# Kernel tuning notes

Hardware: AMD Instinct MI355X
Metric: run time of the kernel (lower is better)

The kernel has to match this reference:

```python
import jax, jax.numpy as jnp
import numpy as np

B, NV, H, W = 4, 1, 224, 224
GH = GW = 16                 # 224 // 14 patch grid
NT = 1 + GH * GW             # 257 tokens (cls + patches)
CIN, DF, DH = 1152, 512, 128
NP0 = 512
UPF = (4, 8)
RADIUS = 1.0


def setup_inputs():
    key = jax.random.key(0)
    ks = jax.random.split(key, 8)
    rn = lambda k, s, sc: jax.random.normal(k, s) * sc
    points = jax.random.uniform(ks[0], (B, NP0, 3), minval=-0.5, maxval=0.5)
    tokens = rn(ks[1], (B, CIN, NT), 0.5)
    # OpenGL-style c2w (the forward flips cols 1:3 to OpenCV); camera at z=+2 looking at origin
    c2w = np.tile(np.eye(4, dtype=np.float32), (B, NV, 1, 1))
    c2w[..., 2, 3] = 2.0
    K = np.zeros((B, NV, 3, 3), dtype=np.float32)
    K[..., 0, 0] = 250.0; K[..., 1, 1] = 250.0
    K[..., 0, 2] = W / 2.0; K[..., 1, 2] = H / 2.0
    K[..., 2, 2] = 1.0
    return dict(
        points=points, input_image_tokens=tokens,
        c2w_cond=jnp.asarray(c2w), intrinsic_cond=jnp.asarray(K),
        w1=rn(ks[2], (2 * DF, CIN), CIN ** -0.5), b1=jnp.zeros((2 * DF,)),
        w2=rn(ks[3], (DF, 2 * DF), (2 * DF) ** -0.5), b2=jnp.zeros((DF,)),
        s0_w1=rn(ks[4], (DH, 3 + DF), (3 + DF) ** -0.5), s0_b1=jnp.zeros((DH,)),
        s0_ow=rn(ks[5], (UPF[0] * 3, DH), DH ** -0.5), s0_ob=jnp.zeros((UPF[0] * 3,)),
        s1_w1=rn(ks[6], (DH, 3 + DF), (3 + DF) ** -0.5), s1_b1=jnp.zeros((DH,)),
        s1_ow=rn(ks[7], (UPF[1] * 3, DH), DH ** -0.5), s1_ob=jnp.zeros((UPF[1] * 3,)))


def _points_projection(pts, c2w, K, lf):
    # pts: (B,N,3), c2w: (B,4,4) OpenCV, K: (B,3,3), lf: (B,C,H,W)
    N = pts.shape[1]
    w2c = jnp.linalg.inv(c2w)
    cam = jnp.einsum('bij,bnj->bni', w2c[:, :3, :3], pts) + w2c[:, None, :3, 3]
    z = cam[..., 2]
    zs = jnp.where(jnp.abs(z) > 1e-8, z, 1e-8)
    px = K[:, 0, 0][:, None] * cam[..., 0] / zs + K[:, 0, 2][:, None]
    py = K[:, 1, 1][:, None] * cam[..., 1] / zs + K[:, 1, 2][:, None]
    ix = jnp.floor(px).astype(jnp.int32)
    iy = jnp.floor(py).astype(jnp.int32)
    valid = (z > 1e-6) & (ix >= 0) & (ix < W) & (iy >= 0) & (iy < H)
    pix = jnp.where(valid, iy * W + ix, H * W)                  # (B,N); dummy bin H*W
    nseg = B * (H * W + 1)
    seg = (jnp.arange(B)[:, None] * (H * W + 1) + pix).reshape(-1)
    zf = jnp.where(valid, z, jnp.inf).reshape(-1)
    minz = jax.ops.segment_min(zf, seg, num_segments=nseg)      # z-buffer (points_per_pixel=1)
    ismin = valid.reshape(-1) & (zf <= minz[seg])
    pid = jnp.arange(B * N)
    win = jax.ops.segment_min(jnp.where(ismin, pid, B * N), seg, num_segments=nseg)
    visible = (pid == win[seg]).reshape(B, N)                   # unique winner per pixel
    lff = lf.reshape(B, -1, H * W)
    g = jnp.take_along_axis(lff, jnp.clip(pix, 0, H * W - 1)[:, None, :], axis=2)  # (B,C,N)
    return jnp.where(visible[:, None, :], g, 0.0)


def reference(points, input_image_tokens, c2w_cond, intrinsic_cond,
              w1, b1, w2, b2, s0_w1, s0_b1, s0_ow, s0_ob, s1_w1, s1_b1, s1_ow, s1_ob):
    # mlp_feat_cond: 1x1 conv MLP over tokens
    feat = jax.nn.relu(jnp.einsum('oc,bcn->bon', w1, input_image_tokens) + b1[:, None])
    feat = jnp.einsum('oc,bcn->bon', w2, feat) + b2[:, None]    # (B, DF, NT)
    # OpenGL -> OpenCV flip of c2w columns 1:3
    flip = jnp.ones((4, 4)).at[:3, 1:3].set(-1.0)
    c2w = c2w_cond[:, 0] * flip
    Kmat = intrinsic_cond[:, 0]
    # drop cls token, to patch grid, bilinear upsample to image resolution
    lf = jnp.transpose(feat, (0, 2, 1))[:, 1:].reshape(B, GH, GW, DF)
    lf = jnp.transpose(lf, (0, 3, 1, 2))
    lf = jax.image.resize(lf, (B, DF, H, W), method='bilinear')  # (B, DF, H, W)
    pts = points
    pcd = jnp.transpose(points, (0, 2, 1))                      # (B,3,N)
    stages = (((s0_w1, s0_b1, s0_ow, s0_ob), UPF[0]), ((s1_w1, s1_b1, s1_ow, s1_ob), UPF[1]))
    outs = []
    for (ws, bs, ow, ob), f in stages:
        up_cond = _points_projection(pts, c2w, Kmat, lf)        # (B, DF, N) visibility-masked gather
        h = jax.nn.relu(jnp.einsum('oc,bcn->bon', ws,
                                   jnp.concatenate([pcd, up_cond], axis=1)) + bs[:, None])
        off = jnp.tanh(jnp.einsum('oc,bcn->bon', ow, h) + ob[:, None])  # (B, 3f, N)
        n = pcd.shape[2]
        off = off.reshape(B, f, 3, n).transpose(0, 2, 3, 1).reshape(B, 3, n * f)
        pcd = jnp.repeat(pcd, f, axis=2) + off * RADIUS         # SPD-style bounded upsample
        pts = jnp.transpose(pcd, (0, 2, 1))
        outs.append(pts)
    return tuple(outs)
```

## Files before the change

kernel.cpp:

```cpp
#include <hip/hip_runtime.h>
#include <hip/hip_bf16.h>
#include <cstdint>
#include <cstddef>

using bf16 = __hip_bfloat16;
typedef __attribute__((ext_vector_type(8))) short bf16x8_t;
typedef __attribute__((ext_vector_type(4))) float f32x4_t;

#define BB 4
#define HH 224
#define WWD 224
#define NTOK 257
#define CINC 1152
#define DFC 512

constexpr size_t OFF_G2    = 256;
constexpr size_t OFF_WC    = OFF_G2;
constexpr size_t OFF_T     = OFF_G2 + 1052672;
constexpr size_t OFF_SCR   = 256 + 2105344;
constexpr size_t OFF_FEAT1 = OFF_SCR;
constexpr size_t OFF_ZBUF  = OFF_SCR;
constexpr size_t OFF_PINFO = OFF_SCR + 1605632;
constexpr size_t WS_NEED   = OFF_SCR + 1736704;
constexpr size_t WS_FULL   = OFF_SCR + 4210688;

__device__ __forceinline__ float ldf(const void* p, size_t i, bool f32) {
  return f32 ? ((const float*)p)[i] : __bfloat162float(((const bf16*)p)[i]);
}
__device__ __forceinline__ double ldd(const void* p, size_t i, bool f32) {
  return f32 ? (double)((const float*)p)[i]
             : (double)__bfloat162float(((const bf16*)p)[i]);
}
__device__ __forceinline__ bool detect_f32(const void* c2w_raw) {
  const float* fc = (const float*)c2w_raw;
  return (fc[0] == 1.0f) && (fc[5] == 1.0f);
}

__device__ void compute_cam(const void* c2w_raw, const void* K_raw, int b, bool f32,
                            double* cw) {
  double m[16];
#pragma unroll
  for (int i = 0; i < 16; ++i) m[i] = ldd(c2w_raw, b*16 + i, f32);
  m[1]=-m[1]; m[2]=-m[2]; m[5]=-m[5]; m[6]=-m[6]; m[9]=-m[9]; m[10]=-m[10];
  double i0  =  m[5]*m[10]*m[15] - m[5]*m[11]*m[14] - m[9]*m[6]*m[15] + m[9]*m[7]*m[14] + m[13]*m[6]*m[11] - m[13]*m[7]*m[10];
  double i4  = -m[4]*m[10]*m[15] + m[4]*m[11]*m[14] + m[8]*m[6]*m[15] - m[8]*m[7]*m[14] - m[12]*m[6]*m[11] + m[12]*m[7]*m[10];
  double i8  =  m[4]*m[9]*m[15]  - m[4]*m[11]*m[13] - m[8]*m[5]*m[15] + m[8]*m[7]*m[13] + m[12]*m[5]*m[11] - m[12]*m[7]*m[9];
  double i12 = -m[4]*m[9]*m[14]  + m[4]*m[10]*m[13] + m[8]*m[5]*m[14] - m[8]*m[6]*m[13] - m[12]*m[5]*m[10] + m[12]*m[6]*m[9];
  double i1  = -m[1]*m[10]*m[15] + m[1]*m[11]*m[14] + m[9]*m[2]*m[15] - m[9]*m[3]*m[14] - m[13]*m[2]*m[11] + m[13]*m[3]*m[10];
  double i5  =  m[0]*m[10]*m[15] - m[0]*m[11]*m[14] - m[8]*m[2]*m[15] + m[8]*m[3]*m[14] + m[12]*m[2]*m[11] - m[12]*m[3]*m[10];
  double i9  = -m[0]*m[9]*m[15]  + m[0]*m[11]*m[13] + m[8]*m[1]*m[15] - m[8]*m[3]*m[13] - m[12]*m[1]*m[11] + m[12]*m[3]*m[9];
  double i13 =  m[0]*m[9]*m[14]  - m[0]*m[10]*m[13] - m[8]*m[1]*m[14] + m[8]*m[2]*m[13] + m[12]*m[1]*m[10] - m[12]*m[2]*m[9];
  double i2  =  m[1]*m[6]*m[15]  - m[1]*m[7]*m[14]  - m[5]*m[2]*m[15] + m[5]*m[3]*m[14] + m[13]*m[2]*m[7]  - m[13]*m[3]*m[6];
  double i6  = -m[0]*m[6]*m[15]  + m[0]*m[7]*m[14]  + m[4]*m[2]*m[15] - m[4]*m[3]*m[14] - m[12]*m[2]*m[7]  + m[12]*m[3]*m[6];
  double i10 =  m[0]*m[5]*m[15]  - m[0]*m[7]*m[13]  - m[4]*m[1]*m[15] + m[4]*m[3]*m[13] + m[12]*m[1]*m[7]  - m[12]*m[3]*m[5];
  double i14 = -m[0]*m[5]*m[14]  + m[0]*m[6]*m[13]  + m[4]*m[1]*m[14] - m[4]*m[2]*m[13] - m[12]*m[1]*m[6]  + m[12]*m[2]*m[5];
  double i3  = -m[1]*m[6]*m[11]  + m[1]*m[7]*m[10]  + m[5]*m[2]*m[11] - m[5]*m[3]*m[10] - m[9]*m[2]*m[7]   + m[9]*m[3]*m[6];
  double i7  =  m[0]*m[6]*m[11]  - m[0]*m[7]*m[10]  - m[4]*m[2]*m[11] + m[4]*m[3]*m[10] + m[8]*m[2]*m[7]   - m[8]*m[3]*m[6];
  double i11 = -m[0]*m[5]*m[11]  + m[0]*m[7]*m[9]   + m[4]*m[1]*m[11] - m[4]*m[3]*m[9]  - m[8]*m[1]*m[7]   + m[8]*m[3]*m[5];
  double det = m[0]*i0 + m[1]*i4 + m[2]*i8 + m[3]*i12;
  double r = 1.0 / det;
  cw[0]=i0*r;  cw[1]=i1*r;  cw[2]=i2*r;  cw[3]=i3*r;
  cw[4]=i4*r;  cw[5]=i5*r;  cw[6]=i6*r;  cw[7]=i7*r;
  cw[8]=i8*r;  cw[9]=i9*r;  cw[10]=i10*r; cw[11]=i11*r;
  cw[12] = ldd(K_raw, b*9+0, f32);
  cw[13] = ldd(K_raw, b*9+2, f32);
  cw[14] = ldd(K_raw, b*9+4, f32);
  cw[15] = ldd(K_raw, b*9+5, f32);
}

template <int XK, int WK, bool TROUT, bool ATOMIC, bool BSTR, int PREC>
__global__ __launch_bounds__(256) void gemm_mfma(
    const void* __restrict__ Wm, const void* __restrict__ Wm2,
    const void* __restrict__ X, const void* __restrict__ xb,
    const float* __restrict__ bstr_p, int bstr,
    float* __restrict__ Y, const void* __restrict__ c2w_raw,
    int O, int K, int Nn, int Yld,
    int bx0, int bxm, int by0, int bym,
    int Wld, int Wc0, int skn) {
  __shared__ __align__(16) short SMEM[6 * 2560];
  short* Whi = SMEM;
  short* Wmd = SMEM + 2560;
  short* Wlo = SMEM + 5120;
  short* Xhi = SMEM + 7680;
  short* Xmd = SMEM + 10240;
  short* Xlo = SMEM + 12800;
  const bool f32 = detect_f32(c2w_raw);
  int tid = threadIdx.x;
  int n0 = blockIdx.x * 64;
  int o0 = blockIdx.y * 64;
  int bz = (int)blockIdx.z;
  int bidx = bz / skn;
  int ks = bz - bidx * skn;
  int bx = bx0 + bxm * bidx;
  int by = by0 + bym * bidx;
  int kq = K / skn;
  int kbase = ks * kq;
  int so  = tid >> 2;
  int skq = tid & 3;
  int sn  = tid & 63;
  int skg = tid >> 6;
  int wv = tid >> 6, lane = tid & 63;
  int lm = lane & 15, lq = lane >> 4;

  float wreg[8], xreg[8];
  f32x4_t acc[4] = {};

  auto load_w = [&](int c0) {
    if constexpr (WK == 3) {
      int orow = o0 + so;
      const void* Wp = (orow < 128) ? Wm : Wm2;
      size_t base = (size_t)(orow & 127) * Wld + Wc0 + c0 + skq * 8;
#pragma unroll
      for (int j = 0; j < 8; ++j) wreg[j] = ldf(Wp, base + j, f32);
    } else if constexpr (WK == 1) {
      const float* Wf = (const float*)Wm;
      size_t base = (size_t)(o0 + so) * Wld + c0 + skq * 8;
      float4 v0 = *(const float4*)(Wf + base);
      float4 v1 = *(const float4*)(Wf + base + 4);
      wreg[0]=v0.x; wreg[1]=v0.y; wreg[2]=v0.z; wreg[3]=v0.w;
      wreg[4]=v1.x; wreg[5]=v1.y; wreg[6]=v1.z; wreg[7]=v1.w;
    } else {
      size_t base = (size_t)(o0 + so) * Wld + c0 + skq * 8;
      if (f32) {
        const float* Wf = (const float*)Wm;
        float4 v0 = *(const float4*)(Wf + base);
        float4 v1 = *(const float4*)(Wf + base + 4);
        wreg[0]=v0.x; wreg[1]=v0.y; wreg[2]=v0.z; wreg[3]=v0.w;
        wreg[4]=v1.x; wreg[5]=v1.y; wreg[6]=v1.z; wreg[7]=v1.w;
      } else {
        const unsigned short* Wh = (const unsigned short*)Wm;
        ushort4 u0 = *(const ushort4*)(Wh + base);
        ushort4 u1 = *(const ushort4*)(Wh + base + 4);
        wreg[0]=__uint_as_float((unsigned)u0.x<<16); wreg[1]=__uint_as_float((unsigned)u0.y<<16);
        wreg[2]=__uint_as_float((unsigned)u0.z<<16); wreg[3]=__uint_as_float((unsigned)u0.w<<16);
        wreg[4]=__uint_as_float((unsigned)u1.x<<16); wreg[5]=__uint_as_float((unsigned)u1.y<<16);
        wreg[6]=__uint_as_float((unsigned)u1.z<<16); wreg[7]=__uint_as_float((unsigned)u1.w<<16);
      }
    }
  };
  auto load_x = [&](int c0) {
    int gn = n0 + sn;
#pragma unroll
    for (int j = 0; j < 8; ++j) {
      int c = c0 + skg * 8 + j;
      float v = 0.f;
      if (gn < Nn) {
        if (XK == 3) {
          v = (gn < 1024) ? ldf(X, (size_t)c * 1024 + gn, f32)
                          : ((gn == 1024) ? ldf(xb, c, f32) : 0.f);
        } else if (XK == 2) {
          size_t xi = ((size_t)bx * K + c) * Nn + gn;
          v = fmaxf(((const float*)X)[xi] + ldf(xb, c, f32), 0.f);
        } else {
          size_t xi = ((size_t)bx * K + c) * Nn + gn;
          v = ldf(X, xi, f32);
        }
      }
      xreg[j] = v;
    }
  };
  auto store_hi = [&](const float* r, short* hp, int off) {
    int hd[4];
#pragma unroll
    for (int d = 0; d < 4; ++d) {
      unsigned b0 = __float_as_uint(r[2*d]), b1 = __float_as_uint(r[2*d+1]);
      hd[d] = (int)((b0 >> 16) | (b1 & 0xFFFF0000u));
    }
    *(int4*)&hp[off] = make_int4(hd[0], hd[1], hd[2], hd[3]);
  };
  auto split_store3 = [&](const float* r, short* hp, short* mp, short* lp, int off) {
    int hd[4], md[4], ld[4];
#pragma unroll
    for (int d = 0; d < 4; ++d) {
      float v0 = r[2*d], v1 = r[2*d+1];
      unsigned b0 = __float_as_uint(v0), b1 = __float_as_uint(v1);
      hd[d] = (int)((b0 >> 16) | (b1 & 0xFFFF0000u));
      float h0 = __uint_as_float(b0 & 0xFFFF0000u);
      float h1 = __uint_as_float(b1 & 0xFFFF0000u);
      float r0 = v0 - h0, r1 = v1 - h1;
      unsigned c0 = __float_as_uint(r0), c1 = __float_as_uint(r1);
      md[d] = (int)((c0 >> 16) | (c1 & 0xFFFF0000u));
      float m0 = __uint_as_float(c0 & 0xFFFF0000u);
      float m1 = __uint_as_float(c1 & 0xFFFF0000u);
      unsigned e0 = __float_as_uint(r0 - m0), e1 = __float_as_uint(r1 - m1);
      ld[d] = (int)((e0 >> 16) | (e1 & 0xFFFF0000u));
    }
    *(int4*)&hp[off] = make_int4(hd[0], hd[1], hd[2], hd[3]);
    *(int4*)&mp[off] = make_int4(md[0], md[1], md[2], md[3]);
    *(int4*)&lp[off] = make_int4(ld[0], ld[1], ld[2], ld[3]);
  };

  int nkt = kq / 32;
  int woff = so * 40 + skq * 8;
  int xoff = sn * 40 + skg * 8;
  int aoff = (wv * 16 + lm) * 40 + lq * 8;
  load_w(kbase); load_x(kbase);

  if (PREC == 0 && !f32) {
    for (int kt = 0; kt < nkt; ++kt) {
      __syncthreads();
      store_hi(wreg, Whi, woff);
      store_hi(xreg, Xhi, xoff);
      __syncthreads();
      if (kt + 1 < nkt) { load_w(kbase + (kt + 1) * 32); load_x(kbase + (kt + 1) * 32); }
      bf16x8_t ahi = *(const bf16x8_t*)&Whi[aoff];
#pragma unroll
      for (int nt = 0; nt < 4; ++nt) {
        int boff = (nt * 16 + lm) * 40 + lq * 8;
        bf16x8_t bhi = *(const bf16x8_t*)&Xhi[boff];
        acc[nt] = __builtin_amdgcn_mfma_f32_16x16x32_bf16(ahi, bhi, acc[nt], 0, 0, 0);
      }
    }
  } else {
    for (int kt = 0; kt < nkt; ++kt) {
      __syncthreads();
      split_store3(wreg, Whi, Wmd, Wlo, woff);
      split_store3(xreg, Xhi, Xmd, Xlo, xoff);
      __syncthreads();
      if (kt + 1 < nkt) { load_w(kbase + (kt + 1) * 32); load_x(kbase + (kt + 1) * 32); }
      bf16x8_t ahi = *(const bf16x8_t*)&Whi[aoff];
      bf16x8_t amd = *(const bf16x8_t*)&Wmd[aoff];
      bf16x8_t alo = *(const bf16x8_t*)&Wlo[aoff];
#pragma unroll
      for (int nt = 0; nt < 4; ++nt) {
        int boff = (nt * 16 + lm) * 40 + lq * 8;
        bf16x8_t bhi = *(const bf16x8_t*)&Xhi[boff];
        bf16x8_t bmd = *(const bf16x8_t*)&Xmd[boff];
        bf16x8_t blo = *(const bf16x8_t*)&Xlo[boff];
        acc[nt] = __builtin_amdgcn_mfma_f32_16x16x32_bf16(ahi, blo, acc[nt], 0, 0, 0);
        acc[nt] = __builtin_amdgcn_mfma_f32_16x16x32_bf16(amd, bmd, acc[nt], 0, 0, 0);
        acc[nt] = __builtin_amdgcn_mfma_f32_16x16x32_bf16(alo, bhi, acc[nt], 0, 0, 0);
        acc[nt] = __builtin_amdgcn_mfma_f32_16x16x32_bf16(amd, bhi, acc[nt], 0, 0, 0);
        acc[nt] = __builtin_amdgcn_mfma_f32_16x16x32_bf16(ahi, bmd, acc[nt], 0, 0, 0);
        acc[nt] = __builtin_amdgcn_mfma_f32_16x16x32_bf16(ahi, bhi, acc[nt], 0, 0, 0);
      }
    }
  }

  if (!ATOMIC) {
#pragma unroll
    for (int nt = 0; nt < 4; ++nt) {
      int gn = n0 + nt * 16 + lm;
      if (gn < Nn) {
#pragma unroll
        for (int r = 0; r < 4; ++r) {
          int o = o0 + wv * 16 + lq * 4 + r;
          size_t yi = TROUT ? ((size_t)by * Nn + gn) * Yld + o
                            : ((size_t)by * O + o) * (size_t)Yld + gn;
          Y[yi] = acc[nt][r];
        }
      }
    }
  } else if (!TROUT) {
#pragma unroll
    for (int nt = 0; nt < 4; ++nt) {
      int gn = n0 + nt * 16 + lm;
      if (gn < Nn) {
#pragma unroll
        for (int r = 0; r < 4; ++r) {
          int o = o0 + wv * 16 + lq * 4 + r;
          float v = acc[nt][r];
          if (BSTR && ks == 0) v += bstr_p[(size_t)o * bstr];
          atomicAdd(&Y[((size_t)by * O + o) * (size_t)Yld + gn], v);
        }
      }
    }
  } else {
    __syncthreads();
    float* ts = (float*)SMEM;
#pragma unroll
    for (int nt = 0; nt < 4; ++nt) {
      int n = nt * 16 + lm;
      int ob = wv * 16 + lq * 4;
#pragma unroll
      for (int r = 0; r < 4; ++r) ts[(ob + r) * 65 + n] = acc[nt][r];
    }
    __syncthreads();
    int oo = tid & 63;
    int nb = tid >> 6;
    float bv = (BSTR && ks == 0) ? bstr_p[(size_t)(o0 + oo) * bstr] : 0.f;
#pragma unroll
    for (int i = 0; i < 16; ++i) {
      int n = nb * 16 + i;
      int gn = n0 + n;
      if (gn < Nn)
        atomicAdd(&Y[((size_t)by * Nn + gn) * (size_t)Yld + o0 + oo],
                  ts[oo * 65 + n] + bv);
    }
  }
}

template <int XK, bool RELU, bool TROUT>
__global__ __launch_bounds__(256) void gemm_k(const void* __restrict__ Wm, const void* __restrict__ X,
                                              const void* __restrict__ bias, float* __restrict__ Y,
                                              const void* __restrict__ c2w_raw, int O, int K, int Nn,
                                              int bx0, int bxm, int by0, int bym) {
  const int TK = 32;
  __shared__ __align__(16) float Ws[TK * 68];
  __shared__ __align__(16) float Xs[TK * 68];
  const bool f32 = detect_f32(c2w_raw);
  int tid = threadIdx.x;
  int n0 = blockIdx.x * 64;
  int o0 = blockIdx.y * 64;
  int bx = bx0 + bxm * (int)blockIdx.z;
  int by = by0 + bym * (int)blockIdx.z;
  int tx = tid & 15, ty = tid >> 4;
  int wo  = tid >> 3;
  int wk4 = tid & 7;
  float acc[4][4] = {};
  float4 wv[2];
  float  xv[8];

  auto load_tile = [&](int c0) {
#pragma unroll
    for (int i = 0; i < 2; ++i) {
      int o = wo + i * 32;
      size_t off = (size_t)(o0 + o) * K + c0 + 4 * wk4;
      if (f32) {
        wv[i] = *(const float4*)((const float*)Wm + off);
      } else {
        ushort4 u = *(const ushort4*)((const unsigned short*)Wm + off);
        wv[i] = make_float4(__uint_as_float((unsigned)u.x << 16),
                            __uint_as_float((unsigned)u.y << 16),
                            __uint_as_float((unsigned)u.z << 16),
                            __uint_as_float((unsigned)u.w << 16));
      }
    }
#pragma unroll
    for (int i = 0; i < 8; ++i) {
      int idx = i * 256 + tid;
      int n = idx & 63, k = idx >> 6;
      int gn = n0 + n;
      float v = 0.f;
      if (gn < Nn) {
        size_t xi = ((size_t)bx * K + c0 + k) * Nn + gn;
        v = (XK == 0) ? ldf(X, xi, f32) : ((const float*)X)[xi];
      }
      xv[i] = v;
    }
  };

  int nkt = K / TK;
  load_tile(0);
  for (int kt = 0; kt < nkt; ++kt) {
    __syncthreads();
#pragma unroll
    for (int i = 0; i < 2; ++i) {
      int o = wo + i * 32;
      Ws[(4 * wk4 + 0) * 68 + o] = wv[i].x;
      Ws[(4 * wk4 + 1) * 68 + o] = wv[i].y;
      Ws[(4 * wk4 + 2) * 68 + o] = wv[i].z;
      Ws[(4 * wk4 + 3) * 68 + o] = wv[i].w;
    }
#pragma unroll
    for (int i = 0; i < 8; ++i) {
      int idx = i * 256 + tid;
      int n = idx & 63, k = idx >> 6;
      Xs[k * 68 + n] = xv[i];
    }
    __syncthreads();
    if (kt + 1 < nkt) load_tile((kt + 1) * TK);
#pragma unroll
    for (int k = 0; k < TK; ++k) {
      const float4 a  = *(const float4*)&Ws[k * 68 + tx * 4];
      const float4 bb = *(const float4*)&Xs[k * 68 + ty * 4];
      acc[0][0] = fmaf(a.x, bb.x, acc[0][0]); acc[0][1] = fmaf(a.x, bb.y, acc[0][1]);
      acc[0][2] = fmaf(a.x, bb.z, acc[0][2]); acc[0][3] = fmaf(a.x, bb.w, acc[0][3]);
      acc[1][0] = fmaf(a.y, bb.x, acc[1][0]); acc[1][1] = fmaf(a.y, bb.y, acc[1][1]);
      acc[1][2] = fmaf(a.y, bb.z, acc[1][2]); acc[1][3] = fmaf(a.y, bb.w, acc[1][3]);
      acc[2][0] = fmaf(a.z, bb.x, acc[2][0]); acc[2][1] = fmaf(a.z, bb.y, acc[2][1]);
      acc[2][2] = fmaf(a.z, bb.z, acc[2][2]); acc[2][3] = fmaf(a.z, bb.w, acc[2][3]);
      acc[3][0] = fmaf(a.w, bb.x, acc[3][0]); acc[3][1] = fmaf(a.w, bb.y, acc[3][1]);
      acc[3][2] = fmaf(a.w, bb.z, acc[3][2]); acc[3][3] = fmaf(a.w, bb.w, acc[3][3]);
    }
  }
#pragma unroll
  for (int oi = 0; oi < 4; ++oi) {
    int o = o0 + tx * 4 + oi;
    float bv = ldf(bias, o, f32);
#pragma unroll
    for (int ni = 0; ni < 4; ++ni) {
      int gn = n0 + ty * 4 + ni;
      if (gn < Nn) {
        float v = acc[oi][ni] + bv;
        if (RELU) v = fmaxf(v, 0.f);
        size_t yi = TROUT ? ((size_t)by * Nn + gn) * O + o
                          : ((size_t)by * O + o) * Nn + gn;
        Y[yi] = v;
      }
    }
  }
}

template <int PMODE>
__global__ __launch_bounds__(256) void proj_k(const void* __restrict__ pts,
                                              const void* __restrict__ c2w_raw,
                                              const void* __restrict__ K_raw,
                                              unsigned long long* __restrict__ zbuf,
                                              int* __restrict__ pinfo, int N) {
  int m = blockIdx.x * 256 + threadIdx.x;
  if (m >= BB * N) return;
  const bool f32 = detect_f32(c2w_raw);
  int b = m / N;
  double cw[16];
  compute_cam(c2w_raw, K_raw, b, f32, cw);
  double px, py, pz;
  if (PMODE == 1) {
    const float* pf = (const float*)pts;
    px = pf[m*3+0]; py = pf[m*3+1]; pz = pf[m*3+2];
  } else {
    px = ldd(pts, (size_t)m*3+0, f32);
    py = ldd(pts, (size_t)m*3+1, f32);
    pz = ldd(pts, (size_t)m*3+2, f32);
  }
  double cx = cw[0]*px + cw[1]*py + cw[2]*pz + cw[3];
  double cy = cw[4]*px + cw[5]*py + cw[6]*pz + cw[7];
  double z  = cw[8]*px + cw[9]*py + cw[10]*pz + cw[11];
  double zs = (fabs(z) > 1e-8) ? z : 1e-8;
  double fpx = cw[12] * cx / zs + cw[13];
  double fpy = cw[14] * cy / zs + cw[15];
  double fix = floor(fpx), fiy = floor(fpy);
  bool valid = (z > 1e-6) && (fix >= 0.0) && (fix < (double)WWD) && (fiy >= 0.0) && (fiy < (double)HH);
  int* pi = pinfo + (size_t)m * 4;
  if (valid) {
    int ix = (int)fix, iy = (int)fiy;
    int zidx = b * (HH * WWD) + iy * WWD + ix;
    float zf = (float)z;
    unsigned long long key = ((unsigned long long)__float_as_uint(zf) << 32) | (unsigned)m;
    atomicMin(&zbuf[zidx], key);
    pi[0] = zidx; pi[1] = 1;
    *(unsigned long long*)(pi + 2) = key;
  } else {
    pi[0] = 0; pi[1] = 0; pi[2] = 0; pi[3] = 0;
  }
}

template <int PMODE, int F, int TM>
__global__ __launch_bounds__(256) void stage2_k(
    const void* __restrict__ pts_in,
    const float* __restrict__ Tm,
    const int* __restrict__ pinfo,
    const unsigned long long* __restrict__ zbuf,
    const void* __restrict__ w1,
    const void* __restrict__ b1,
    const void* __restrict__ ow,
    const void* __restrict__ ob,
    const void* __restrict__ c2w_raw,
    float* __restrict__ out,
    int N) {
  constexpr int TPP = 256 / TM;
  constexpr int OC  = 128 / TPP;
  __shared__ int   ro_s[TM * 4];
  __shared__ float wt_s[TM * 4];
  __shared__ float p_s[TM * 3];
  __shared__ float Wp_s[128 * 3];
  __shared__ float b1_s[128];
  __shared__ __align__(16) float ow_s[F * 3 * 132];
  __shared__ __align__(16) float Hs[TM * 132];

  const bool f32 = detect_f32(c2w_raw);
  int tid = threadIdx.x;
  int m0 = blockIdx.x * TM;

  if (tid < TM) {
    int m = m0 + tid;
    const int* pi = pinfo + (size_t)m * 4;
    int zidx = pi[0];
    unsigned long long key = *(const unsigned long long*)(pi + 2);
    bool vis = pi[1] && (zbuf[zidx] == key);
    float s = vis ? 1.f : 0.f;
    int b = m / N;
    int rem = zidx - b * (HH * WWD);
    int iy = rem / WWD, ix = rem - iy * WWD;
    float sx = fminf(fmaxf(((float)ix + 0.5f) / 14.0f - 0.5f, 0.f), 15.f);
    float sy = fminf(fmaxf(((float)iy + 0.5f) / 14.0f - 0.5f, 0.f), 15.f);
    int x0 = (int)sx, y0 = (int)sy;
    int x1 = min(x0 + 1, 15), y1 = min(y0 + 1, 15);
    float fx = sx - (float)x0, fy = sy - (float)y0;
    int base = b * NTOK;
    ro_s[tid*4+0] = (base + 1 + y0*16 + x0) * 256;
    ro_s[tid*4+1] = (base + 1 + y0*16 + x1) * 256;
    ro_s[tid*4+2] = (base + 1 + y1*16 + x0) * 256;
    ro_s[tid*4+3] = (base + 1 + y1*16 + x1) * 256;
    wt_s[tid*4+0] = s * (1.f-fy)*(1.f-fx);
    wt_s[tid*4+1] = s * (1.f-fy)*fx;
    wt_s[tid*4+2] = s * fy*(1.f-fx);
    wt_s[tid*4+3] = s * fy*fx;
#pragma unroll
    for (int d = 0; d < 3; ++d) {
      p_s[tid*3 + d] = (PMODE == 1) ? ((const float*)pts_in)[(size_t)m*3 + d]
                                    : ldf(pts_in, (size_t)m*3 + d, f32);
    }
  }
  for (int i = tid; i < 128 * 3; i += 256) Wp_s[i] = ldf(w1, (size_t)(i / 3) * 515 + (i % 3), f32);
  for (int i = tid; i < 128; i += 256) b1_s[i] = ldf(b1, i, f32);
  for (int i = tid; i < F * 3 * 128; i += 256) ow_s[(i >> 7) * 132 + (i & 127)] = ldf(ow, i, f32);
  __syncthreads();

  {
    int pt = tid / TPP;
    int tx = tid % TPP;
    int oc0 = tx * OC;
    const float* t0p = Tm + ro_s[pt*4+0] + oc0;
    const float* t1p = Tm + ro_s[pt*4+1] + oc0;
    const float* t2p = Tm + ro_s[pt*4+2] + oc0;
    const float* t3p = Tm + ro_s[pt*4+3] + oc0;
    float w0 = wt_s[pt*4+0], w1v = wt_s[pt*4+1], w2v = wt_s[pt*4+2], w3v = wt_s[pt*4+3];
    float px = p_s[pt*3+0], py = p_s[pt*3+1], pz = p_s[pt*3+2];
#pragma unroll
    for (int i = 0; i < OC; i += 4) {
      f32x4_t c0 = *(const f32x4_t*)(t0p + i);
      f32x4_t c1 = *(const f32x4_t*)(t1p + i);
      f32x4_t c2 = *(const f32x4_t*)(t2p + i);
      f32x4_t c3 = *(const f32x4_t*)(t3p + i);
      f32x4_t hv;
#pragma unroll
      for (int j = 0; j < 4; ++j) {
        int o = oc0 + i + j;
        float v = b1_s[o]
                + Wp_s[o*3+0]*px + Wp_s[o*3+1]*py + Wp_s[o*3+2]*pz
                + w0*c0[j] + w1v*c1[j] + w2v*c2[j] + w3v*c3[j];
        hv[j] = fmaxf(v, 0.f);
      }
      *(f32x4_t*)&Hs[pt * 132 + oc0 + i] = hv;
    }
  }
  __syncthreads();

  const int tasks = TM * F * 3;
  for (int t = tid; t < tasks; t += 256) {
    int mI = t % TM;
    int r  = t / TM;
    f32x4_t acc4 = {0.f, 0.f, 0.f, 0.f};
#pragma unroll
    for (int k = 0; k < 128; k += 4) {
      f32x4_t hv = *(const f32x4_t*)&Hs[mI * 132 + k];
      f32x4_t wv = *(const f32x4_t*)&ow_s[r * 132 + k];
      acc4 += hv * wv;
    }
    float dot = acc4[0] + acc4[1] + acc4[2] + acc4[3] + ldf(ob, r, f32);
    float val = tanhf(dot);
    int j = r / 3, d = r - j * 3;
    int m = m0 + mI;
    out[((size_t)m * F + j) * 3 + d] = p_s[mI * 3 + d] + val;
  }
}

template <int PMODE, int F>
__global__ __launch_bounds__(256) void stage_k(
    const void* __restrict__ pts_in,
    const float* __restrict__ g2,
    const int* __restrict__ pinfo,
    const unsigned long long* __restrict__ zbuf,
    const void* __restrict__ w1,
    const void* __restrict__ b1,
    const void* __restrict__ ow,
    const void* __restrict__ ob,
    const void* __restrict__ c2w_raw,
    float* __restrict__ out,
    int N) {
  const int TM = 16, TK = 32;
  __shared__ int   ro_s[TM * 4];
  __shared__ float wt_s[TM * 4];
  __shared__ float p_s[TM * 3];
  __shared__ float ow_s[F * 3 * 128];
  __shared__ __align__(16) float uni[4800];
  float* Ws = uni;
  float* Vs = uni + 4224;
  float* Hs = uni;

  const bool f32 = detect_f32(c2w_raw);
  int tid = threadIdx.x;
  int m0 = blockIdx.x * TM;

  if (tid < TM) {
    int m = m0 + tid;
    const int* pi = pinfo + (size_t)m * 4;
    int zidx = pi[0];
    unsigned long long key = *(const unsigned long long*)(pi + 2);
    bool vis = pi[1] && (zbuf[zidx] == key);
    float s = vis ? 1.f : 0.f;
    int b = m / N;
    int rem = zidx - b * (HH * WWD);
    int iy = rem / WWD, ix = rem - iy * WWD;
    float sx = fminf(fmaxf(((float)ix + 0.5f) / 14.0f - 0.5f, 0.f), 15.f);
    float sy = fminf(fmaxf(((float)iy + 0.5f) / 14.0f - 0.5f, 0.f), 15.f);
    int x0 = (int)sx, y0 = (int)sy;
    int x1 = min(x0 + 1, 15), y1 = min(y0 + 1, 15);
    float fx = sx - (float)x0, fy = sy - (float)y0;
    int base = b * NTOK;
    ro_s[tid*4+0] = (base + 1 + y0*16 + x0) * DFC;
    ro_s[tid*4+1] = (base + 1 + y0*16 + x1) * DFC;
    ro_s[tid*4+2] = (base + 1 + y1*16 + x0) * DFC;
    ro_s[tid*4+3] = (base + 1 + y1*16 + x1) * DFC;
    wt_s[tid*4+0] = s * (1.f-fy)*(1.f-fx);
    wt_s[tid*4+1] = s * (1.f-fy)*fx;
    wt_s[tid*4+2] = s * fy*(1.f-fx);
    wt_s[tid*4+3] = s * fy*fx;
#pragma unroll
    for (int d = 0; d < 3; ++d) {
      p_s[tid*3 + d] = (PMODE == 1) ? ((const float*)pts_in)[(size_t)m*3 + d]
                                    : ldf(pts_in, (size_t)m*3 + d, f32);
    }
  }
  for (int i = tid; i < F * 3 * 128; i += 256) ow_s[i] = ldf(ow, i, f32);
  __syncthreads();

  int tx = tid & 15, ty = tid >> 4;
  float acc[2][4] = {};
  float wreg[16];
  float greg[2][4];
  float vbase[2];

  auto prefetch = [&](int c0) {
    if (f32) {
      const float* w1f = (const float*)w1;
#pragma unroll
      for (int i = 0; i < 16; ++i) {
        int idx = i * 256 + tid;
        int k = idx & 31, o = idx >> 5;
        int c = c0 + k;
        wreg[i] = (c < 515) ? w1f[(size_t)o * 515 + c] : 0.f;
      }
    } else {
      const bf16* w1h = (const bf16*)w1;
#pragma unroll
      for (int i = 0; i < 16; ++i) {
        int idx = i * 256 + tid;
        int k = idx & 31, o = idx >> 5;
        int c = c0 + k;
        wreg[i] = (c < 515) ? __bfloat162float(w1h[(size_t)o * 515 + c]) : 0.f;
      }
    }
#pragma unroll
    for (int i = 0; i < 2; ++i) {
      int idx = i * 256 + tid;
      int mI = idx & 15, k = idx >> 4;
      int c = c0 + k;
      vbase[i] = 0.f;
      greg[i][0] = greg[i][1] = greg[i][2] = greg[i][3] = 0.f;
      if (c < 3) {
        vbase[i] = p_s[mI*3 + c];
      } else if (c < 515) {
        int ch = c - 3;
        greg[i][0] = g2[ro_s[mI*4+0] + ch];
        greg[i][1] = g2[ro_s[mI*4+1] + ch];
        greg[i][2] = g2[ro_s[mI*4+2] + ch];
        greg[i][3] = g2[ro_s[mI*4+3] + ch];
      }
    }
  };

  prefetch(0);
  for (int kt = 0; kt < 17; ++kt) {
    __syncthreads();
#pragma unroll
    for (int i = 0; i < 16; ++i) {
      int idx = i * 256 + tid;
      int k = idx & 31, o = idx >> 5;
      Ws[k * 132 + o] = wreg[i];
    }
#pragma unroll
    for (int i = 0; i < 2; ++i) {
      int idx = i * 256 + tid;
      int mI = idx & 15, k = idx >> 4;
      Vs[k * 18 + mI] = vbase[i]
        + wt_s[mI*4+0] * greg[i][0] + wt_s[mI*4+1] * greg[i][1]
        + wt_s[mI*4+2] * greg[i][2] + wt_s[mI*4+3] * greg[i][3];
    }
    __syncthreads();
    if (kt + 1 < 17) prefetch((kt + 1) * TK);
#pragma unroll
    for (int k = 0; k < TK; ++k) {
      const float4 a0 = *(const float4*)&Ws[k * 132 + tx * 4];
      const float4 a1 = *(const float4*)&Ws[k * 132 + 64 + tx * 4];
      const float  bb = Vs[k * 18 + ty];
      acc[0][0] = fmaf(a0.x, bb, acc[0][0]);
      acc[0][1] = fmaf(a0.y, bb, acc[0][1]);
      acc[0][2] = fmaf(a0.z, bb, acc[0][2]);
      acc[0][3] = fmaf(a0.w, bb, acc[0][3]);
      acc[1][0] = fmaf(a1.x, bb, acc[1][0]);
      acc[1][1] = fmaf(a1.y, bb, acc[1][1]);
      acc[1][2] = fmaf(a1.z, bb, acc[1][2]);
      acc[1][3] = fmaf(a1.w, bb, acc[1][3]);
    }
  }
  __syncthreads();
#pragma unroll
  for (int h = 0; h < 2; ++h) {
#pragma unroll
    for (int oi = 0; oi < 4; ++oi) {
      int o = h * 64 + tx * 4 + oi;
      float bv = ldf(b1, o, f32);
      Hs[o * 18 + ty] = fmaxf(acc[h][oi] + bv, 0.f);
    }
  }
  __syncthreads();
  const int tasks = TM * F * 3;
  for (int t = tid; t < tasks; t += 256) {
    int mI = t & 15, r = t >> 4;
    float dot = ldf(ob, r, f32);
#pragma unroll 8
    for (int k = 0; k < 128; ++k) dot = fmaf(ow_s[r * 128 + k], Hs[k * 18 + mI], dot);
    float val = tanhf(dot);
    int j = r / 3, d = r - j * 3;
    int m = m0 + mI;
    out[((size_t)m * F + j) * 3 + d] = p_s[mI * 3 + d] + val;
  }
}

extern "C" void kernel_launch(void* const* d_in, const int* in_sizes, int n_in,
                              void* d_out, int out_size, void* d_ws, size_t ws_size,
                              hipStream_t stream) {
  const void* points = d_in[0];
  const void* tokens = d_in[1];
  const void* c2w    = d_in[2];
  const void* intr   = d_in[3];
  const void* w1     = d_in[4];
  const void* b1     = d_in[5];
  const void* w2     = d_in[6];
  const void* b2     = d_in[7];
  const void* s0w1   = d_in[8];
  const void* s0b1   = d_in[9];
  const void* s0ow   = d_in[10];
  const void* s0ob   = d_in[11];
  const void* s1w1   = d_in[12];
  const void* s1b1   = d_in[13];
  const void* s1ow   = d_in[14];
  const void* s1ob   = d_in[15];

  if (ws_size < WS_NEED) {
    hipMemsetAsync(d_out, 0, (size_t)out_size * sizeof(float), stream);
    return;
  }

  char* ws = (char*)d_ws;
  unsigned long long* zbuf = (unsigned long long*)(ws + OFF_ZBUF);
  int* pinfo    = (int*)(ws + OFF_PINFO);
  float* out    = (float*)d_out;
  float* out0   = out;
  float* out1   = out + 24576;

  const int NB = (NTOK + 63) / 64;
  const size_t zbytes = (size_t)BB * HH * WWD * 8;

  if (ws_size >= WS_FULL) {
    float* Wc    = (float*)(ws + OFF_WC);
    float* Tb    = (float*)(ws + OFF_T);
    float* feat1 = (float*)(ws + OFF_FEAT1);

    hipMemsetAsync(ws + OFF_WC, 0, 2105344, stream);
    hipMemsetAsync(feat1, 0, 4210688, stream);

    gemm_mfma<3, 3, false, true, false, 0><<<dim3(17, 4, 4), 256, 0, stream>>>(
        s0w1, s1w1, w2, b2, nullptr, 0, Wc, c2w,
        256, 512, 1025, 1028, 0, 0, 0, 0, 515, 3, 4);

    gemm_mfma<0, 0, false, true, false, 0><<<dim3(NB, 16, 12), 256, 0, stream>>>(
        w1, nullptr, tokens, nullptr, nullptr, 0, feat1, c2w,
        1024, CINC, NTOK, NTOK, 0, 1, 0, 1, CINC, 0, 3);

    gemm_mfma<2, 1, true, true, true, 1><<<dim3(NB, 4, 32), 256, 0, stream>>>(
        Wc, nullptr, feat1, b1, Wc + 1024, 1028, Tb, c2w,
        256, 1024, NTOK, 256, 0, 1, 0, 1, 1028, 0, 8);

    hipMemsetAsync(zbuf, 0xFF, zbytes, stream);
    proj_k<0><<<(BB * 512) / 256, 256, 0, stream>>>(points, c2w, intr, zbuf, pinfo, 512);
    stage2_k<0, 4, 8><<<(BB * 512) / 8, 256, 0, stream>>>(points, Tb, pinfo, zbuf,
                                                          s0w1, s0b1, s0ow, s0ob, c2w,
                                                          out0, 512);
    hipMemsetAsync(zbuf, 0xFF, zbytes, stream);
    proj_k<1><<<(BB * 2048) / 256, 256, 0, stream>>>(out0, c2w, intr, zbuf, pinfo, 2048);
    stage2_k<1, 8, 8><<<(BB * 2048) / 8, 256, 0, stream>>>(out0, Tb + 128, pinfo, zbuf,
                                                           s1w1, s1b1, s1ow, s1ob, c2w,
                                                           out1, 2048);
  } else {
    float* g2    = (float*)(ws + OFF_G2);
    float* feat1 = (float*)(ws + OFF_FEAT1);
    for (int b = 0; b < BB; ++b) {
      gemm_k<0, true, false><<<dim3(NB, 16, 1), 256, 0, stream>>>(
          w1, tokens, b1, feat1, c2w, 1024, CINC, NTOK, b, 0, 0, 0);
      gemm_k<1, false, true><<<dim3(NB, 8, 1), 256, 0, stream>>>(
          w2, feat1, b2, g2, c2w, 512, 1024, NTOK, 0, 0, b, 0);
    }
    hipMemsetAsync(zbuf, 0xFF, zbytes, stream);
    proj_k<0><<<(BB * 512) / 256, 256, 0, stream>>>(points, c2w, intr, zbuf, pinfo, 512);
    stage_k<0, 4><<<(BB * 512) / 16, 256, 0, stream>>>(points, g2, pinfo, zbuf,
                                                       s0w1, s0b1, s0ow, s0ob, c2w,
                                                       out0, 512);
    hipMemsetAsync(zbuf, 0xFF, zbytes, stream);
    proj_k<1><<<(BB * 2048) / 256, 256, 0, stream>>>(out0, c2w, intr, zbuf, pinfo, 2048);
    stage_k<1, 8><<<(BB * 2048) / 16, 256, 0, stream>>>(out0, g2, pinfo, zbuf,
                                                        s1w1, s1b1, s1ow, s1ob, c2w,
                                                        out1, 2048);
  }
}
```

Measured before the change: 218.0 us.

## Pre-split fp32 operands into bf16 triples once and merge memsets

```diff
diff --git a/kernel.cpp b/kernel.cpp
--- a/kernel.cpp
+++ b/kernel.cpp
@@ -14,15 +14,19 @@
 #define CINC 1152
 #define DFC 512
 
-constexpr size_t OFF_G2    = 256;
-constexpr size_t OFF_WC    = OFF_G2;
-constexpr size_t OFF_T     = OFF_G2 + 1052672;
-constexpr size_t OFF_SCR   = 256 + 2105344;
-constexpr size_t OFF_FEAT1 = OFF_SCR;
-constexpr size_t OFF_ZBUF  = OFF_SCR;
-constexpr size_t OFF_PINFO = OFF_SCR + 1605632;
-constexpr size_t WS_NEED   = OFF_SCR + 1736704;
-constexpr size_t WS_FULL   = OFF_SCR + 4210688;
+constexpr size_t OFF_WC     = 256;
+constexpr size_t OFF_T      = OFF_WC + 1052672;
+constexpr size_t OFF_SCR    = 256 + 2105344;
+constexpr size_t OFF_FEAT1  = OFF_SCR;
+constexpr size_t OFF_FLO    = OFF_SCR + 4210688;
+constexpr size_t OFF_WLO    = OFF_FLO + 2105344;
+constexpr size_t OFF_ZB0    = OFF_WLO + 526336;
+constexpr size_t OFF_ZB1    = OFF_ZB0 + 1605632;
+constexpr size_t OFF_PINFO2 = OFF_ZB1 + 1605632;
+constexpr size_t WS_FULL2   = OFF_PINFO2 + 131072;
+constexpr size_t OFF_ZBUF   = OFF_SCR;
+constexpr size_t OFF_PINFO  = OFF_SCR + 1605632;
+constexpr size_t WS_NEED    = OFF_SCR + 1736704;
 
 __device__ __forceinline__ float ldf(const void* p, size_t i, bool f32) {
   return f32 ? ((const float*)p)[i] : __bfloat162float(((const bf16*)p)[i]);
@@ -34,6 +38,16 @@
 __device__ __forceinline__ bool detect_f32(const void* c2w_raw) {
   const float* fc = (const float*)c2w_raw;
   return (fc[0] == 1.0f) && (fc[5] == 1.0f);
+}
+__device__ __forceinline__ void split3(float x, unsigned& hm, unsigned short& lo) {
+  unsigned b = __float_as_uint(x);
+  float h = __uint_as_float(b & 0xFFFF0000u);
+  float r = x - h;
+  unsigned c = __float_as_uint(r);
+  float m = __uint_as_float(c & 0xFFFF0000u);
+  float e = r - m;
+  hm = (b >> 16) | (c & 0xFFFF0000u);
+  lo = (unsigned short)(__float_as_uint(e) >> 16);
 }
 
 __device__ void compute_cam(const void* c2w_raw, const void* K_raw, int b, bool f32,
@@ -103,10 +117,24 @@
   int lm = lane & 15, lq = lane >> 4;
 
   float wreg[8], xreg[8];
+  unsigned wpk[8], xpk[8];
+  unsigned short wlo8[8], xlo8[8];
   f32x4_t acc[4] = {};
 
   auto load_w = [&](int c0) {
-    if constexpr (WK == 3) {
+    if constexpr (PREC == 3) {
+      const unsigned* WH = (const unsigned*)Wm;
+      const unsigned short* WL = (const unsigned short*)Wm2;
+      size_t base = (size_t)(o0 + so) * Wld + c0 + skq * 8;
+      uint4 a = *(const uint4*)(WH + base);
+      uint4 b = *(const uint4*)(WH + base + 4);
+      wpk[0]=a.x; wpk[1]=a.y; wpk[2]=a.z; wpk[3]=a.w;
+      wpk[4]=b.x; wpk[5]=b.y; wpk[6]=b.z; wpk[7]=b.w;
+      ushort4 l0 = *(const ushort4*)(WL + base);
+      ushort4 l1 = *(const ushort4*)(WL + base + 4);
+      wlo8[0]=l0.x; wlo8[1]=l0.y; wlo8[2]=l0.z; wlo8[3]=l0.w;
+      wlo8[4]=l1.x; wlo8[5]=l1.y; wlo8[6]=l1.z; wlo8[7]=l1.w;
+    } else if constexpr (WK == 3) {
       int orow = o0 + so;
       const void* Wp = (orow < 128) ? Wm : Wm2;
       size_t base = (size_t)(orow & 127) * Wld + Wc0 + c0 + skq * 8;
@@ -140,23 +168,35 @@
   };
   auto load_x = [&](int c0) {
     int gn = n0 + sn;
-#pragma unroll
-    for (int j = 0; j < 8; ++j) {
-      int c = c0 + skg * 8 + j;
-      float v = 0.f;
-      if (gn < Nn) {
-        if (XK == 3) {
-          v = (gn < 1024) ? ldf(X, (size_t)c * 1024 + gn, f32)
-                          : ((gn == 1024) ? ldf(xb, c, f32) : 0.f);
-        } else if (XK == 2) {
-          size_t xi = ((size_t)bx * K + c) * Nn + gn;
-          v = fmaxf(((const float*)X)[xi] + ldf(xb, c, f32), 0.f);
-        } else {
-          size_t xi = ((size_t)bx * K + c) * Nn + gn;
-          v = ldf(X, xi, f32);
+    if constexpr (PREC == 3) {
+      const unsigned* XH = (const unsigned*)X;
+      const unsigned short* XL = (const unsigned short*)xb;
+#pragma unroll
+      for (int j = 0; j < 8; ++j) {
+        int c = c0 + skg * 8 + j;
+        size_t xi = ((size_t)bx * K + c) * Nn + gn;
+        xpk[j]  = (gn < Nn) ? XH[xi] : 0u;
+        xlo8[j] = (gn < Nn) ? XL[xi] : (unsigned short)0;
+      }
+    } else {
+#pragma unroll
+      for (int j = 0; j < 8; ++j) {
+        int c = c0 + skg * 8 + j;
+        float v = 0.f;
+        if (gn < Nn) {
+          if (XK == 3) {
+            v = (gn < 1024) ? ldf(X, (size_t)c * 1024 + gn, f32)
+                            : ((gn == 1024) ? ldf(xb, c, f32) : 0.f);
+          } else if (XK == 2) {
+            size_t xi = ((size_t)bx * K + c) * Nn + gn;
+            v = fmaxf(((const float*)X)[xi] + ldf(xb, c, f32), 0.f);
+          } else {
+            size_t xi = ((size_t)bx * K + c) * Nn + gn;
+            v = ldf(X, xi, f32);
+          }
         }
-      }
-      xreg[j] = v;
+        xreg[j] = v;
+      }
     }
   };
   auto store_hi = [&](const float* r, short* hp, int off) {
@@ -167,6 +207,24 @@
       hd[d] = (int)((b0 >> 16) | (b1 & 0xFFFF0000u));
     }
     *(int4*)&hp[off] = make_int4(hd[0], hd[1], hd[2], hd[3]);
+  };
+  auto store_hm = [&](const unsigned* p, short* hp, short* mp, int off) {
+    int hd[4], md[4];
+#pragma unroll
+    for (int d = 0; d < 4; ++d) {
+      unsigned a = p[2*d], b = p[2*d+1];
+      hd[d] = (int)((a & 0xFFFFu) | (b << 16));
+      md[d] = (int)((a >> 16) | (b & 0xFFFF0000u));
+    }
+    *(int4*)&hp[off] = make_int4(hd[0], hd[1], hd[2], hd[3]);
+    *(int4*)&mp[off] = make_int4(md[0], md[1], md[2], md[3]);
+  };
+  auto store_lo16 = [&](const unsigned short* p, short* lp, int off) {
+    int ld[4];
+#pragma unroll
+    for (int d = 0; d < 4; ++d)
+      ld[d] = (int)((unsigned)p[2*d] | ((unsigned)p[2*d+1] << 16));
+    *(int4*)&lp[off] = make_int4(ld[0], ld[1], ld[2], ld[3]);
   };
   auto split_store3 = [&](const float* r, short* hp, short* mp, short* lp, int off) {
     int hd[4], md[4], ld[4];
@@ -196,26 +254,13 @@
   int aoff = (wv * 16 + lm) * 40 + lq * 8;
   load_w(kbase); load_x(kbase);
 
-  if (PREC == 0 && !f32) {
+  if constexpr (PREC == 3) {
     for (int kt = 0; kt < nkt; ++kt) {
       __syncthreads();
-      store_hi(wreg, Whi, woff);
-      store_hi(xreg, Xhi, xoff);
-      __syncthreads();
-      if (kt + 1 < nkt) { load_w(kbase + (kt + 1) * 32); load_x(kbase + (kt + 1) * 32); }
-      bf16x8_t ahi = *(const bf16x8_t*)&Whi[aoff];
-#pragma unroll
-      for (int nt = 0; nt < 4; ++nt) {
-        int boff = (nt * 16 + lm) * 40 + lq * 8;
-        bf16x8_t bhi = *(const bf16x8_t*)&Xhi[boff];
-        acc[nt] = __builtin_amdgcn_mfma_f32_16x16x32_bf16(ahi, bhi, acc[nt], 0, 0, 0);
-      }
-    }
-  } else {
-    for (int kt = 0; kt < nkt; ++kt) {
-      __syncthreads();
-      split_store3(wreg, Whi, Wmd, Wlo, woff);
-      split_store3(xreg, Xhi, Xmd, Xlo, xoff);
+      store_hm(wpk, Whi, Wmd, woff);
+      store_lo16(wlo8, Wlo, woff);
+      store_hm(xpk, Xhi, Xmd, xoff);
+      store_lo16(xlo8, Xlo, xoff);
       __syncthreads();
       if (kt + 1 < nkt) { load_w(kbase + (kt + 1) * 32); load_x(kbase + (kt + 1) * 32); }
       bf16x8_t ahi = *(const bf16x8_t*)&Whi[aoff];
@@ -235,7 +280,57 @@
         acc[nt] = __builtin_amdgcn_mfma_f32_16x16x32_bf16(ahi, bhi, acc[nt], 0, 0, 0);
       }
     }
-  }
+  } else if (PREC == 0 && !f32) {
+    for (int kt = 0; kt < nkt; ++kt) {
+      __syncthreads();
+      store_hi(wreg, Whi, woff);
+      store_hi(xreg, Xhi, xoff);
+      __syncthreads();
+      if (kt + 1 < nkt) { load_w(kbase + (kt + 1) * 32); load_x(kbase + (kt + 1) * 32); }
+      bf16x8_t ahi = *(const bf16x8_t*)&Whi[aoff];
+#pragma unroll
+      for (int nt = 0; nt < 4; ++nt) {
+        int boff = (nt * 16 + lm) * 40 + lq * 8;
+        bf16x8_t bhi = *(const bf16x8_t*)&Xhi[boff];
+        acc[nt] = __builtin_amdgcn_mfma_f32_16x16x32_bf16(ahi, bhi, acc[nt], 0, 0, 0);
+      }
+    }
+  } else {
+    for (int kt = 0; kt < nkt; ++kt) {
+      __syncthreads();
+      split_store3(wreg, Whi, Wmd, Wlo, woff);
+      split_store3(xreg, Xhi, Xmd, Xlo, xoff);
+      __syncthreads();
+      if (kt + 1 < nkt) { load_w(kbase + (kt + 1) * 32); load_x(kbase + (kt + 1) * 32); }
+      bf16x8_t ahi = *(const bf16x8_t*)&Whi[aoff];
+      bf16x8_t amd = *(const bf16x8_t*)&Wmd[aoff];
+      bf16x8_t alo = *(const bf16x8_t*)&Wlo[aoff];
+#pragma unroll
+      for (int nt = 0; nt < 4; ++nt) {
+        int boff = (nt * 16 + lm) * 40 + lq * 8;
+        bf16x8_t bhi = *(const bf16x8_t*)&Xhi[boff];
+        bf16x8_t bmd = *(const bf16x8_t*)&Xmd[boff];
+        bf16x8_t blo = *(const bf16x8_t*)&Xlo[boff];
+        acc[nt] = __builtin_amdgcn_mfma_f32_16x16x32_bf16(ahi, blo, acc[nt], 0, 0, 0);
+        acc[nt] = __builtin_amdgcn_mfma_f32_16x16x32_bf16(amd, bmd, acc[nt], 0, 0, 0);
+        acc[nt] = __builtin_amdgcn_mfma_f32_16x16x32_bf16(alo, bhi, acc[nt], 0, 0, 0);
+        acc[nt] = __builtin_amdgcn_mfma_f32_16x16x32_bf16(amd, bhi, acc[nt], 0, 0, 0);
+        acc[nt] = __builtin_amdgcn_mfma_f32_16x16x32_bf16(ahi, bmd, acc[nt], 0, 0, 0);
+        acc[nt] = __builtin_amdgcn_mfma_f32_16x16x32_bf16(ahi, bhi, acc[nt], 0, 0, 0);
+      }
+    }
+  }
+
+  auto bload = [&](int o) -> float {
+    if constexpr (PREC == 3) {
+      unsigned p = ((const unsigned*)Wm)[(size_t)o * Wld + 1024];
+      unsigned short pl = ((const unsigned short*)Wm2)[(size_t)o * Wld + 1024];
+      return __uint_as_float(p << 16) + __uint_as_float(p & 0xFFFF0000u)
+           + __uint_as_float((unsigned)pl << 16);
+    } else {
+      return bstr_p[(size_t)o * bstr];
+    }
+  };
 
   if (!ATOMIC) {
 #pragma unroll
@@ -260,7 +355,7 @@
         for (int r = 0; r < 4; ++r) {
           int o = o0 + wv * 16 + lq * 4 + r;
           float v = acc[nt][r];
-          if (BSTR && ks == 0) v += bstr_p[(size_t)o * bstr];
+          if (BSTR && ks == 0) v += bload(o);
           atomicAdd(&Y[((size_t)by * O + o) * (size_t)Yld + gn], v);
         }
       }
@@ -278,7 +373,7 @@
     __syncthreads();
     int oo = tid & 63;
     int nb = tid >> 6;
-    float bv = (BSTR && ks == 0) ? bstr_p[(size_t)(o0 + oo) * bstr] : 0.f;
+    float bv = (BSTR && ks == 0) ? bload(o0 + oo) : 0.f;
 #pragma unroll
     for (int i = 0; i < 16; ++i) {
       int n = nb * 16 + i;
@@ -287,6 +382,37 @@
         atomicAdd(&Y[((size_t)by * Nn + gn) * (size_t)Yld + o0 + oo],
                   ts[oo * 65 + n] + bv);
     }
+  }
+}
+
+__global__ __launch_bounds__(256) void presplit3_k(
+    float* __restrict__ feat, const void* __restrict__ b1,
+    float* __restrict__ wc,
+    unsigned short* __restrict__ flo, unsigned short* __restrict__ wlo,
+    const void* __restrict__ c2w_raw) {
+  const int NFE = BB * 1024 * NTOK;
+  const bool f32 = detect_f32(c2w_raw);
+  int i4 = (blockIdx.x * 256 + threadIdx.x) * 4;
+  unsigned hm[4]; unsigned short lo[4];
+  if (i4 < NFE) {
+    float4 v = *(const float4*)(feat + i4);
+    float e[4] = {v.x, v.y, v.z, v.w};
+#pragma unroll
+    for (int j = 0; j < 4; ++j) {
+      int k = ((i4 + j) / NTOK) & 1023;
+      e[j] = fmaxf(e[j] + ldf(b1, k, f32), 0.f);
+      split3(e[j], hm[j], lo[j]);
+    }
+    *(uint4*)(feat + i4) = make_uint4(hm[0], hm[1], hm[2], hm[3]);
+    *(ushort4*)(flo + i4) = make_ushort4(lo[0], lo[1], lo[2], lo[3]);
+  } else {
+    int j0 = i4 - NFE;
+    float4 v = *(const float4*)(wc + j0);
+    float e[4] = {v.x, v.y, v.z, v.w};
+#pragma unroll
+    for (int j = 0; j < 4; ++j) split3(e[j], hm[j], lo[j]);
+    *(uint4*)(wc + j0) = make_uint4(hm[0], hm[1], hm[2], hm[3]);
+    *(ushort4*)(wlo + j0) = make_ushort4(lo[0], lo[1], lo[2], lo[3]);
   }
 }
 
@@ -735,8 +861,6 @@
   }
 
   char* ws = (char*)d_ws;
-  unsigned long long* zbuf = (unsigned long long*)(ws + OFF_ZBUF);
-  int* pinfo    = (int*)(ws + OFF_PINFO);
   float* out    = (float*)d_out;
   float* out0   = out;
   float* out1   = out + 24576;
@@ -744,39 +868,47 @@
   const int NB = (NTOK + 63) / 64;
   const size_t zbytes = (size_t)BB * HH * WWD * 8;
 
-  if (ws_size >= WS_FULL) {
+  if (ws_size >= WS_FULL2) {
     float* Wc    = (float*)(ws + OFF_WC);
     float* Tb    = (float*)(ws + OFF_T);
     float* feat1 = (float*)(ws + OFF_FEAT1);
-
-    hipMemsetAsync(ws + OFF_WC, 0, 2105344, stream);
-    hipMemsetAsync(feat1, 0, 4210688, stream);
+    unsigned short* flo = (unsigned short*)(ws + OFF_FLO);
+    unsigned short* wlo = (unsigned short*)(ws + OFF_WLO);
+    unsigned long long* zb0 = (unsigned long long*)(ws + OFF_ZB0);
+    unsigned long long* zb1 = (unsigned long long*)(ws + OFF_ZB1);
+    int* pinfo = (int*)(ws + OFF_PINFO2);
+
+    hipMemsetAsync(ws + OFF_WC, 0, 6316032, stream);
+    hipMemsetAsync(ws + OFF_ZB0, 0xFF, 2 * zbytes, stream);
 
     gemm_mfma<3, 3, false, true, false, 0><<<dim3(17, 4, 4), 256, 0, stream>>>(
         s0w1, s1w1, w2, b2, nullptr, 0, Wc, c2w,
         256, 512, 1025, 1028, 0, 0, 0, 0, 515, 3, 4);
 
-    gemm_mfma<0, 0, false, true, false, 0><<<dim3(NB, 16, 12), 256, 0, stream>>>(
+    gemm_mfma<0, 0, false, true, false, 0><<<dim3(NB, 16, 24), 256, 0, stream>>>(
         w1, nullptr, tokens, nullptr, nullptr, 0, feat1, c2w,
-        1024, CINC, NTOK, NTOK, 0, 1, 0, 1, CINC, 0, 3);
-
-    gemm_mfma<2, 1, true, true, true, 1><<<dim3(NB, 4, 32), 256, 0, stream>>>(
-        Wc, nullptr, feat1, b1, Wc + 1024, 1028, Tb, c2w,
+        1024, CINC, NTOK, NTOK, 0, 1, 0, 1, CINC, 0, 6);
+
+    presplit3_k<<<(BB * 1024 * NTOK + 256 * 1028) / 1024, 256, 0, stream>>>(
+        feat1, b1, Wc, flo, wlo, c2w);
+
+    gemm_mfma<5, 5, true, true, true, 3><<<dim3(NB, 4, 32), 256, 0, stream>>>(
+        Wc, wlo, feat1, flo, nullptr, 0, Tb, c2w,
         256, 1024, NTOK, 256, 0, 1, 0, 1, 1028, 0, 8);
 
-    hipMemsetAsync(zbuf, 0xFF, zbytes, stream);
-    proj_k<0><<<(BB * 512) / 256, 256, 0, stream>>>(points, c2w, intr, zbuf, pinfo, 512);
-    stage2_k<0, 4, 8><<<(BB * 512) / 8, 256, 0, stream>>>(points, Tb, pinfo, zbuf,
+    proj_k<0><<<(BB * 512) / 256, 256, 0, stream>>>(points, c2w, intr, zb0, pinfo, 512);
+    stage2_k<0, 4, 8><<<(BB * 512) / 8, 256, 0, stream>>>(points, Tb, pinfo, zb0,
                                                           s0w1, s0b1, s0ow, s0ob, c2w,
                                                           out0, 512);
-    hipMemsetAsync(zbuf, 0xFF, zbytes, stream);
-    proj_k<1><<<(BB * 2048) / 256, 256, 0, stream>>>(out0, c2w, intr, zbuf, pinfo, 2048);
-    stage2_k<1, 8, 8><<<(BB * 2048) / 8, 256, 0, stream>>>(out0, Tb + 128, pinfo, zbuf,
+    proj_k<1><<<(BB * 2048) / 256, 256, 0, stream>>>(out0, c2w, intr, zb1, pinfo, 2048);
+    stage2_k<1, 8, 8><<<(BB * 2048) / 8, 256, 0, stream>>>(out0, Tb + 128, pinfo, zb1,
                                                            s1w1, s1b1, s1ow, s1ob, c2w,
                                                            out1, 2048);
   } else {
-    float* g2    = (float*)(ws + OFF_G2);
+    float* g2    = (float*)(ws + OFF_WC);
     float* feat1 = (float*)(ws + OFF_FEAT1);
+    unsigned long long* zbuf = (unsigned long long*)(ws + OFF_ZBUF);
+    int* pinfo = (int*)(ws + OFF_PINFO);
     for (int b = 0; b < BB; ++b) {
       gemm_k<0, true, false><<<dim3(NB, 16, 1), 256, 0, stream>>>(
           w1, tokens, b1, feat1, c2w, 1024, CINC, NTOK, b, 0, 0, 0);
```

New measurement: 221.8 us. No clear change (+1.8%).
